# Optimization experiments

Measured on AMD Instinct MI355X. Metric: run time of the kernel, lower is better.

Reference implementation:

```python
import jax, jax.numpy as jnp
import numpy as np

EPS_PDIST = 1e-8  # torch PairwiseDistance adds eps to (x1 - x2)


def setup_inputs() -> dict:
    key = jax.random.key(0)
    B, T, D = 8, 4096, 256
    student_output = jax.random.normal(key, (B, T, D), dtype=jnp.float32)
    return {"student_output": student_output}


def reference(student_output) -> jnp.ndarray:
    x = student_output.astype(jnp.float32)  # autocast disabled -> fp32
    B, T, D = x.shape
    eps = 1e-8  # forward default arg
    # pairwise inner products [B, T, T]
    dots = jnp.einsum('btd,bsd->bts', x, x)
    # fill diagonal with -1 so a point is never its own NN
    diag = jnp.eye(T, dtype=bool)
    dots = jnp.where(diag[None, :, :], jnp.float32(-1.0), dots)
    I = jnp.argmax(dots, axis=2)  # [B, T] int
    # gather nearest neighbors: neighbors[b, t] = x[b, I[b, t]]
    neighbors = jnp.take_along_axis(x, I[:, :, None], axis=1)  # [B, T, D]
    # PairwiseDistance(2, eps=1e-8): ||x - y + eps||_2
    diff = x - neighbors + EPS_PDIST
    distances = jnp.sqrt(jnp.sum(diff * diff, axis=-1))  # [B, T]
    loss = -jnp.mean(jnp.log(distances + eps))
    return loss
```

## Files before the change

kernel.cpp:

```cpp
#include <hip/hip_runtime.h>
#include <math.h>


#define Bq 8
#define Tq 4096
#define Dq 256
#define TW 32
#define NT 32
#define S_QUART 1024
#define WTILEB (TW * 256)
#define BIAS 256.0f
#define SCL 0x7F7F7F7F

typedef __attribute__((ext_vector_type(4))) int i32x4;
typedef __attribute__((ext_vector_type(8))) int i32x8;
typedef __attribute__((ext_vector_type(16))) float f32x16;
typedef unsigned int u32;

__device__ __forceinline__ void gload_lds16(const void* g, void* l) {
    typedef __attribute__((address_space(1))) const unsigned int gu32;
    typedef __attribute__((address_space(3))) unsigned int lu32;
    __builtin_amdgcn_global_load_lds((gu32*)g, (lu32*)l, 16, 0, 0);
}

__device__ __forceinline__ i32x8 pack32B(i32x4 lo, i32x4 hi) {
    return __builtin_shufflevector(lo, hi, 0, 1, 2, 3, 4, 5, 6, 7);
}

__global__ void cvt_kernel(const float* __restrict__ x, uint2* __restrict__ xq,
                           u32* __restrict__ keys, float* __restrict__ out) {
    const int i = blockIdx.x * blockDim.x + threadIdx.x;
    const float4* in = (const float4*)x;
    float4 v0 = in[2 * i], v1 = in[2 * i + 1];
    u32 a = 0, b = 0, c = 0, d = 0;
    asm volatile("v_cvt_pk_fp8_f32 %0, %1, %2" : "+v"(a) : "v"(v0.x), "v"(v0.y));
    asm volatile("v_cvt_pk_fp8_f32 %0, %1, %2" : "+v"(b) : "v"(v0.z), "v"(v0.w));
    asm volatile("v_cvt_pk_fp8_f32 %0, %1, %2" : "+v"(c) : "v"(v1.x), "v"(v1.y));
    asm volatile("v_cvt_pk_fp8_f32 %0, %1, %2" : "+v"(d) : "v"(v1.z), "v"(v1.w));
    uint2 o;
    o.x = (a & 0xffffu) | (b << 16);
    o.y = (c & 0xffffu) | (d << 16);
    xq[i] = o;
    if (i < Bq * Tq) keys[i] = 0;
    if (i == 0) *out = 0.f;
}

__global__ __launch_bounds__(512, 2)
void argmax_kernel(const unsigned char* __restrict__ xq, u32* __restrict__ keys) {
    const int bid   = blockIdx.x;
    const int batch = bid & 7;
    const int rt    = (bid >> 3) & 7;
    const int sq    = bid >> 6;
    const int tid   = threadIdx.x;
    const int lane  = tid & 63;
    const int wave  = tid >> 6;
    const int l31   = lane & 31;
    const int lh    = lane >> 5;

    const unsigned char* xB = xq + (size_t)batch * Tq * Dq;
    const int rowBase = rt * 512 + wave * 64;
    const int sBase = sq * S_QUART;

    __shared__ char smem[8 * 2 * WTILEB];
    char* myl = smem + wave * (2 * WTILEB);

    i32x8 afrag[4][2];
#pragma unroll
    for (int rb = 0; rb < 2; ++rb) {
        const unsigned char* rp = xB + (size_t)(rowBase + rb * 32 + l31) * Dq + lh * 32;
#pragma unroll
        for (int kc = 0; kc < 4; ++kc)
            afrag[kc][rb] = pack32B(*(const i32x4*)(rp + kc * 64),
                                    *(const i32x4*)(rp + kc * 64 + 16));
    }

    int g_off[8];
#pragma unroll
    for (int it = 0; it < 8; ++it) {
        const int ls = it * 1024 + lane * 16;
        const int s_local = ls >> 8;
        const int q = ls & 255;
        g_off[it] = s_local * 256 + (q ^ ((s_local & 15) << 4));
    }
    int dsoff0[4], dsoff1[4];
    {
        const int mask = (l31 & 15) << 4;
#pragma unroll
        for (int kc = 0; kc < 4; ++kc) {
            const int q = kc * 64 + lh * 32;
            dsoff0[kc] = l31 * 256 + (q ^ mask);
            dsoff1[kc] = l31 * 256 + ((q + 16) ^ mask);
        }
    }

    auto STAGE = [&](int t, int buf) {
        const unsigned char* gsrc = xB + (size_t)(sBase + t * TW) * 256;
        char* lb = myl + buf * WTILEB;
#pragma unroll
        for (int it = 0; it < 8; ++it)
            gload_lds16(gsrc + g_off[it], lb + it * 1024 + lane * 16);
    };

    u32 bkey[2][16];
#pragma unroll
    for (int rb = 0; rb < 2; ++rb)
#pragma unroll
        for (int r = 0; r < 16; ++r) bkey[rb][r] = 0u;

    STAGE(0, 0);
    asm volatile("s_waitcnt vmcnt(0)" ::: "memory");
    __builtin_amdgcn_sched_barrier(0);

    for (int t = 0; t < NT; ++t) {
        if (t + 1 < NT) {
            STAGE(t + 1, (t + 1) & 1);
            asm volatile("s_waitcnt vmcnt(8)" ::: "memory");
        } else {
            asm volatile("s_waitcnt vmcnt(0)" ::: "memory");
        }
        __builtin_amdgcn_sched_barrier(0);

        const char* lb = myl + (t & 1) * WTILEB;

        f32x16 acc[2];
#pragma unroll
        for (int rb = 0; rb < 2; ++rb)
#pragma unroll
            for (int r = 0; r < 16; ++r) acc[rb][r] = BIAS;

#pragma unroll
        for (int kc = 0; kc < 4; ++kc) {
            const i32x8 bfr = pack32B(*(const i32x4*)(lb + dsoff0[kc]),
                                      *(const i32x4*)(lb + dsoff1[kc]));
            acc[0] = __builtin_amdgcn_mfma_scale_f32_32x32x64_f8f6f4(
                afrag[kc][0], bfr, acc[0], 0, 0, 0, SCL, 0, SCL);
            acc[1] = __builtin_amdgcn_mfma_scale_f32_32x32x64_f8f6f4(
                afrag[kc][1], bfr, acc[1], 0, 0, 0, SCL, 0, SCL);
        }

        const int colB = sBase + t * TW;
        const int sv = colB + l31;
        const u32 invs = (u32)(~sv) & 0xFFFu;
        if (colB < rowBase + 64 && rowBase < colB + 32) {
#pragma unroll
            for (int rb = 0; rb < 2; ++rb) {
#pragma unroll
                for (int r = 0; r < 16; ++r) {
                    const int tj = rowBase + rb * 32 + (r & 3) + 8 * (r >> 2) + 4 * lh;
                    u32 key = (__float_as_uint(acc[rb][r]) & ~0xFFFu) | invs;
                    key = (sv == tj) ? 0u : key;
                    bkey[rb][r] = max(bkey[rb][r], key);
                }
            }
        } else {
#pragma unroll
            for (int rb = 0; rb < 2; ++rb) {
#pragma unroll
                for (int r = 0; r < 16; ++r) {
                    const u32 key = (__float_as_uint(acc[rb][r]) & ~0xFFFu) | invs;
                    bkey[rb][r] = max(bkey[rb][r], key);
                }
            }
        }
    }

#pragma unroll
    for (int rb = 0; rb < 2; ++rb) {
#pragma unroll
        for (int r = 0; r < 16; ++r) {
            u32 k = bkey[rb][r];
#pragma unroll
            for (int m = 16; m >= 1; m >>= 1)
                k = max(k, (u32)__shfl_xor((int)k, m, 64));
            if (l31 == 0) {
                const int row = rowBase + rb * 32 + (r & 3) + 8 * (r >> 2) + 4 * lh;
                atomicMax(keys + batch * Tq + row, k);
            }
        }
    }
}

__global__ void loss_kernel(const float* __restrict__ x, const u32* __restrict__ keys,
                            float* __restrict__ out) {
    const int lane = threadIdx.x & 63;
    const int wave = threadIdx.x >> 6;
    const int gw = blockIdx.x * 4 + wave;
    float lsum = 0.f;

    for (int row = gw; row < Bq * Tq; row += 2048) {
        const int b = row >> 12;
        const int t = row & (Tq - 1);
        const int s = (int)((~keys[row]) & 0xFFFu);
        const float4* xt = (const float4*)(x + ((size_t)b * Tq + t) * Dq);
        const float4* xs = (const float4*)(x + ((size_t)b * Tq + s) * Dq);
        float4 a = xt[lane];
        float4 c = xs[lane];
        float dx = a.x - c.x + 1e-8f;
        float dy = a.y - c.y + 1e-8f;
        float dz = a.z - c.z + 1e-8f;
        float dw = a.w - c.w + 1e-8f;
        float sum = dx * dx + dy * dy + dz * dz + dw * dw;
#pragma unroll
        for (int m = 32; m >= 1; m >>= 1)
            sum += __shfl_xor(sum, m, 64);
        if (lane == 0)
            lsum += logf(sqrtf(sum) + 1e-8f);
    }

    __shared__ float red[4];
    if (lane == 0) red[wave] = lsum;
    __syncthreads();
    if (threadIdx.x == 0) {
        float s = red[0] + red[1] + red[2] + red[3];
        atomicAdd(out, -s * (1.0f / (Bq * Tq)));
    }
}

extern "C" void kernel_launch(void* const* d_in, const int* in_sizes, int n_in,
                              void* d_out, int out_size, void* d_ws, size_t ws_size,
                              hipStream_t stream) {
    const float* x = (const float*)d_in[0];
    float* out = (float*)d_out;

    unsigned char* xq = (unsigned char*)d_ws;
    u32* keys = (u32*)((char*)d_ws + (size_t)Bq * Tq * Dq);

    const int n8 = Bq * Tq * Dq / 8;
    cvt_kernel<<<n8 / 256, 256, 0, stream>>>(x, (uint2*)xq, keys, out);
    argmax_kernel<<<256, 512, 0, stream>>>(xq, keys);
    loss_kernel<<<512, 256, 0, stream>>>(x, keys, out);
}
```

Before: 71.22 us.

## Share s-tiles across waves in block-cooperative LDS staging for argmax

Restructures the argmax kernel so the eight waves form a 4x2 grid over 256 rows and a shared 64-column s-tile, loaded cooperatively into LDS, instead of each wave streaming its own private tiles. This is meant to cut redundant global/LDS fill traffic by sharing B-operand tiles across waves. It also changes the grid decomposition to 16 row tiles by 2 s-halves. In exchange it adds a block-wide barrier plus full vmcnt wait every iteration, which can stall waves.

```diff
diff --git a/kernel.cpp b/kernel.cpp
--- a/kernel.cpp
+++ b/kernel.cpp
@@ -5,10 +5,10 @@
 #define Bq 8
 #define Tq 4096
 #define Dq 256
-#define TW 32
-#define NT 32
-#define S_QUART 1024
-#define WTILEB (TW * 256)
+#define SBLK 64
+#define NST 32
+#define S_HALF 2048
+#define TILEB (SBLK * 256)
 #define BIAS 256.0f
 #define SCL 0x7F7F7F7F
 
@@ -49,20 +49,22 @@
 void argmax_kernel(const unsigned char* __restrict__ xq, u32* __restrict__ keys) {
     const int bid   = blockIdx.x;
     const int batch = bid & 7;
-    const int rt    = (bid >> 3) & 7;
-    const int sq    = bid >> 6;
+    const int rt    = (bid >> 3) & 15;
+    const int sh    = bid >> 7;
     const int tid   = threadIdx.x;
     const int lane  = tid & 63;
     const int wave  = tid >> 6;
+    const int waveM = wave >> 1;
+    const int waveN = wave & 1;
     const int l31   = lane & 31;
     const int lh    = lane >> 5;
 
     const unsigned char* xB = xq + (size_t)batch * Tq * Dq;
-    const int rowBase = rt * 512 + wave * 64;
-    const int sBase = sq * S_QUART;
-
-    __shared__ char smem[8 * 2 * WTILEB];
-    char* myl = smem + wave * (2 * WTILEB);
+    const int rowBase = rt * 256 + waveM * 64;
+    const int sHalfBase = sh * S_HALF;
+    const int colOff = waveN * 32;
+
+    __shared__ char smem[2 * TILEB];
 
     i32x8 afrag[4][2];
 #pragma unroll
@@ -74,31 +76,32 @@
                                     *(const i32x4*)(rp + kc * 64 + 16));
     }
 
-    int g_off[8];
-#pragma unroll
-    for (int it = 0; it < 8; ++it) {
-        const int ls = it * 1024 + lane * 16;
+    int g_off[2];
+#pragma unroll
+    for (int it = 0; it < 2; ++it) {
+        const int ls = it * 8192 + tid * 16;
         const int s_local = ls >> 8;
         const int q = ls & 255;
         g_off[it] = s_local * 256 + (q ^ ((s_local & 15) << 4));
     }
     int dsoff0[4], dsoff1[4];
     {
-        const int mask = (l31 & 15) << 4;
+        const int brow = colOff + l31;
+        const int mask = (brow & 15) << 4;
 #pragma unroll
         for (int kc = 0; kc < 4; ++kc) {
             const int q = kc * 64 + lh * 32;
-            dsoff0[kc] = l31 * 256 + (q ^ mask);
-            dsoff1[kc] = l31 * 256 + ((q + 16) ^ mask);
-        }
-    }
-
-    auto STAGE = [&](int t, int buf) {
-        const unsigned char* gsrc = xB + (size_t)(sBase + t * TW) * 256;
-        char* lb = myl + buf * WTILEB;
-#pragma unroll
-        for (int it = 0; it < 8; ++it)
-            gload_lds16(gsrc + g_off[it], lb + it * 1024 + lane * 16);
+            dsoff0[kc] = brow * 256 + (q ^ mask);
+            dsoff1[kc] = brow * 256 + ((q + 16) ^ mask);
+        }
+    }
+
+    auto STAGE = [&](int st, int buf) {
+        const unsigned char* gsrc = xB + (size_t)(sHalfBase + st * SBLK) * 256;
+        char* lb = smem + buf * TILEB;
+#pragma unroll
+        for (int it = 0; it < 2; ++it)
+            gload_lds16(gsrc + g_off[it], lb + it * 8192 + tid * 16);
     };
 
     u32 bkey[2][16];
@@ -108,19 +111,15 @@
         for (int r = 0; r < 16; ++r) bkey[rb][r] = 0u;
 
     STAGE(0, 0);
-    asm volatile("s_waitcnt vmcnt(0)" ::: "memory");
-    __builtin_amdgcn_sched_barrier(0);
-
-    for (int t = 0; t < NT; ++t) {
-        if (t + 1 < NT) {
-            STAGE(t + 1, (t + 1) & 1);
-            asm volatile("s_waitcnt vmcnt(8)" ::: "memory");
-        } else {
-            asm volatile("s_waitcnt vmcnt(0)" ::: "memory");
-        }
-        __builtin_amdgcn_sched_barrier(0);
-
-        const char* lb = myl + (t & 1) * WTILEB;
+    asm volatile("s_waitcnt vmcnt(0)");
+    __syncthreads();
+
+    for (int st = 0; st < NST; ++st) {
+        const int buf = st & 1;
+        if (st + 1 < NST) STAGE(st + 1, buf ^ 1);
+
+        const char* lb = smem + buf * TILEB;
+        const int S0 = sHalfBase + st * SBLK;
 
         f32x16 acc[2];
 #pragma unroll
@@ -138,10 +137,10 @@
                 afrag[kc][1], bfr, acc[1], 0, 0, 0, SCL, 0, SCL);
         }
 
-        const int colB = sBase + t * TW;
-        const int sv = colB + l31;
+        const int colW = S0 + colOff;
+        const int sv = colW + l31;
         const u32 invs = (u32)(~sv) & 0xFFFu;
-        if (colB < rowBase + 64 && rowBase < colB + 32) {
+        if (colW < rowBase + 64 && rowBase < colW + 32) {
 #pragma unroll
             for (int rb = 0; rb < 2; ++rb) {
 #pragma unroll
@@ -162,6 +161,9 @@
                 }
             }
         }
+
+        asm volatile("s_waitcnt vmcnt(0)");
+        __syncthreads();
     }
 
 #pragma unroll
```

New measurement: 68.26 us (median of 3 runs). 4.2% less time.
